# Kernel optimization log

Measured on AMD Instinct MI355X. Metric: run time of the kernel, lower is better.

The kernel has to match this reference:

```python
import jax, jax.numpy as jnp
import numpy as np

DEPTH = 6
HEADS = 4
DH = 64
MAXLEN = 512

def layer_norm(x, s, b, eps=1e-5):
    m = jnp.mean(x, axis=-1, keepdims=True)
    v = jnp.var(x, axis=-1, keepdims=True)
    return (x - m) / jnp.sqrt(v + eps) * s + b

def setup_inputs() -> dict:
    key = jax.random.key(0)
    ks = jax.random.split(key, 8)
    D = 256
    inner = HEADS * DH  # 256
    hid = 1024          # int(256 * 4.0)
    init = lambda k, shape: jax.random.normal(k, shape, jnp.float32) * 0.02
    return {
        "x": jax.random.normal(ks[0], (8, 12, 512, 256), jnp.float32),
        "ln1_s": jnp.ones((DEPTH, D), jnp.float32), "ln1_b": jnp.zeros((DEPTH, D), jnp.float32),
        "qkv_w": init(ks[1], (DEPTH, D, 3 * inner)), "qkv_b": jnp.zeros((DEPTH, 3 * inner), jnp.float32),
        "proj_w": init(ks[2], (DEPTH, inner, D)), "proj_b": jnp.zeros((DEPTH, D), jnp.float32),
        "rel_table": init(ks[3], (DEPTH, 2 * MAXLEN - 1, HEADS)),
        "ln2_s": jnp.ones((DEPTH, D), jnp.float32), "ln2_b": jnp.zeros((DEPTH, D), jnp.float32),
        "w1": init(ks[4], (DEPTH, D, hid)), "b1": jnp.zeros((DEPTH, hid), jnp.float32),
        "w2": init(ks[5], (DEPTH, hid, D)), "b2": jnp.zeros((DEPTH, D), jnp.float32),
        "lnf_s": jnp.ones((D,), jnp.float32), "lnf_b": jnp.zeros((D,), jnp.float32),
    }

def reference(x, ln1_s, ln1_b, qkv_w, qkv_b, proj_w, proj_b, rel_table,
              ln2_s, ln2_b, w1, b1, w2, b2, lnf_s, lnf_b):
    B, L, N, D = x.shape
    h = x.reshape(B * L, N, D)  # (b l) n d
    idx = jnp.arange(N)
    rel_idx = idx[:, None] - idx[None, :] + MAXLEN - 1  # (N, N) in [0, 2*MAXLEN-2]
    scale = DH ** -0.5
    for d in range(DEPTH):
        # pre-norm attention with relative position bias
        xn = layer_norm(h, ln1_s[d], ln1_b[d])
        qkv = xn @ qkv_w[d] + qkv_b[d]
        q, k, v = jnp.split(qkv, 3, axis=-1)
        split_heads = lambda t: t.reshape(B * L, N, HEADS, DH).transpose(0, 2, 1, 3)
        q, k, v = split_heads(q), split_heads(k), split_heads(v)
        bias = rel_table[d][rel_idx].transpose(2, 0, 1)  # (H, N, N)
        scores = jnp.einsum('bhid,bhjd->bhij', q, k) * scale + bias[None]
        attn = jax.nn.softmax(scores, axis=-1)
        o = jnp.einsum('bhij,bhjd->bhid', attn, v)
        o = o.transpose(0, 2, 1, 3).reshape(B * L, N, HEADS * DH)
        h = h + (o @ proj_w[d] + proj_b[d])
        # pre-norm FFN
        xn2 = layer_norm(h, ln2_s[d], ln2_b[d])
        h = h + (jax.nn.gelu(xn2 @ w1[d] + b1[d]) @ w2[d] + b2[d])
    h = layer_norm(h, lnf_s, lnf_b)
    return h.reshape(B, L, N, D)
```

## Files before the change

### kernel.cpp

```cpp
#include <hip/hip_runtime.h>
#include <math.h>

#define T_TOK 49152
#define DMODEL 256
#define NSEQ 512
#define BLROWS 96

typedef unsigned short ushortT;
using frag_ab = __attribute__((ext_vector_type(8))) short;
using f32x4   = __attribute__((ext_vector_type(4))) float;

__device__ __forceinline__ ushortT f2b(float f) {
    union { float f; unsigned int u; } v; v.f = f;
    unsigned int u = v.u;
    u += 0x7FFFu + ((u >> 16) & 1u);
    return (ushortT)(u >> 16);
}
__device__ __forceinline__ float b2f(ushortT h) {
    union { unsigned int u; float f; } v; v.u = ((unsigned int)h) << 16;
    return v.f;
}

__device__ __forceinline__ void gload_lds16(const ushortT* g, ushortT* l) {
    __builtin_amdgcn_global_load_lds(
        (const __attribute__((address_space(1))) unsigned int*)g,
        (__attribute__((address_space(3))) unsigned int*)l, 16, 0, 0);
}

__global__ __launch_bounds__(256) void wprep_kernel(const float* __restrict__ qkv_w,
                                                    const float* __restrict__ proj_w,
                                                    const float* __restrict__ w1,
                                                    const float* __restrict__ w2,
                                                    ushortT* __restrict__ out) {
    __shared__ float Ls[64][132];
    int bid = blockIdx.x;
    int d = bid / 96, t = bid % 96;
    const float* src; int N, KS; size_t dbase; int tt;
    if (t < 24)      { src = qkv_w  + (size_t)d * 256 * 768;  N = 768;  KS = 4;  dbase = (size_t)d * 196608;            tt = t;      }
    else if (t < 32) { src = proj_w + (size_t)d * 256 * 256;  N = 256;  KS = 4;  dbase = 1179648 + (size_t)d * 65536;   tt = t - 24; }
    else if (t < 64) { src = w1     + (size_t)d * 256 * 1024; N = 1024; KS = 4;  dbase = 1572864 + (size_t)d * 262144;  tt = t - 32; }
    else             { src = w2     + (size_t)d * 1024 * 256; N = 256;  KS = 16; dbase = 3145728 + (size_t)d * 262144;  tt = t - 64; }
    int nb = tt / KS, ks = tt % KS;
    int k0 = ks * 64, n0 = nb * 128;
    int tid = threadIdx.x;
#pragma unroll
    for (int i = 0; i < 8; ++i) {
        int fidx = tid + i * 256;
        int kk = fidx >> 5, ng = fidx & 31;
        float4 v = *(const float4*)(src + (size_t)(k0 + kk) * N + n0 + ng * 4);
        *(float4*)&Ls[kk][ng * 4] = v;
    }
    __syncthreads();
    int n = tid & 127, kh = tid >> 7;
    ushortT* dst = out + dbase + (size_t)tt * 8192 + n * 64 + kh * 32;
    ushortT tmp[32];
#pragma unroll
    for (int j = 0; j < 32; ++j) tmp[j] = f2b(Ls[kh * 32 + j][n]);
#pragma unroll
    for (int u = 0; u < 4; ++u) *(uint4*)(dst + u * 8) = *(uint4*)(tmp + u * 8);
}

template <bool OB>
__global__ __launch_bounds__(256) void ln_kernel(const float* __restrict__ in,
                                                 void* __restrict__ out,
                                                 const float* __restrict__ s,
                                                 const float* __restrict__ b) {
    int wave = threadIdx.x >> 6;
    int lane = threadIdx.x & 63;
    size_t row = (size_t)blockIdx.x * 4 + wave;
    float4 v = reinterpret_cast<const float4*>(in + row * DMODEL)[lane];
    float sum = v.x + v.y + v.z + v.w;
    float ssq = v.x * v.x + v.y * v.y + v.z * v.z + v.w * v.w;
#pragma unroll
    for (int m = 1; m <= 32; m <<= 1) {
        sum += __shfl_xor(sum, m, 64);
        ssq += __shfl_xor(ssq, m, 64);
    }
    float mean = sum * (1.0f / 256.0f);
    float var = ssq * (1.0f / 256.0f) - mean * mean;
    float rstd = rsqrtf(var + 1e-5f);
    float4 sv = reinterpret_cast<const float4*>(s)[lane];
    float4 bv = reinterpret_cast<const float4*>(b)[lane];
    float o0 = (v.x - mean) * rstd * sv.x + bv.x;
    float o1 = (v.y - mean) * rstd * sv.y + bv.y;
    float o2 = (v.z - mean) * rstd * sv.z + bv.z;
    float o3 = (v.w - mean) * rstd * sv.w + bv.w;
    if (OB) {
        ushortT* po = (ushortT*)out + row * DMODEL + lane * 4;
        ushort4 ov; ov.x = f2b(o0); ov.y = f2b(o1); ov.z = f2b(o2); ov.w = f2b(o3);
        *(ushort4*)po = ov;
    } else {
        float4 ov; ov.x = o0; ov.y = o1; ov.z = o2; ov.w = o3;
        reinterpret_cast<float4*>((float*)out + row * DMODEL)[lane] = ov;
    }
}

template <int EPI>
__global__ __launch_bounds__(256) void gemm_bf16(const ushortT* __restrict__ A,
                                                 const ushortT* __restrict__ Wt,
                                                 const float* __restrict__ bias,
                                                 float* __restrict__ R,
                                                 ushortT* __restrict__ Cb,
                                                 int K, int N) {
    __shared__ ushortT smem[32768];
    const int nb = blockIdx.x, n0 = nb * 128;
    const int m0 = blockIdx.y * 128;
    const int tid = threadIdx.x, lane = tid & 63, wave = tid >> 6;
    const int wr = wave >> 1, wc = wave & 1;
    const int KS = K >> 6;
    const size_t wtile = (size_t)nb * KS * 8192;

    const int rA = lane >> 3;
    const int colsw = (lane & 7) ^ rA;

    auto STAGE = [&](int buf, int kt) {
        ushortT* Ad = smem + buf * 16384;
        ushortT* Bd = Ad + 8192;
#pragma unroll
        for (int c2 = 0; c2 < 4; ++c2) {
            int rb = wave * 32 + c2 * 8;
            int row = rb + rA;
            gload_lds16(A + (size_t)(m0 + row) * K + kt * 64 + colsw * 8,
                        Ad + rb * 64);
            gload_lds16(Wt + wtile + (size_t)kt * 8192 + row * 64 + colsw * 8,
                        Bd + rb * 64);
        }
    };

    f32x4 acc[4][4];
#pragma unroll
    for (int i = 0; i < 4; ++i)
#pragma unroll
        for (int j = 0; j < 4; ++j) acc[i][j] = (f32x4)0.0f;

    STAGE(0, 0);
    __syncthreads();
    int cur = 0;
    for (int kt = 0; kt < KS; ++kt) {
        if (kt + 1 < KS) STAGE(cur ^ 1, kt + 1);
        const ushortT* Ab = smem + cur * 16384;
        const ushortT* Bb = Ab + 8192;
#pragma unroll
        for (int kst = 0; kst < 2; ++kst) {
            frag_ab af[4], bf4[4];
            int ku = kst * 4 + (lane >> 4);
#pragma unroll
            for (int f = 0; f < 4; ++f) {
                int row = wr * 64 + f * 16 + (lane & 15);
                af[f] = *(const frag_ab*)&Ab[row * 64 + ((ku ^ (row & 7)) << 3)];
                int col = wc * 64 + f * 16 + (lane & 15);
                bf4[f] = *(const frag_ab*)&Bb[col * 64 + ((ku ^ (col & 7)) << 3)];
            }
#pragma unroll
            for (int mf = 0; mf < 4; ++mf)
#pragma unroll
                for (int nf = 0; nf < 4; ++nf)
                    acc[mf][nf] = __builtin_amdgcn_mfma_f32_16x16x32_bf16(
                        af[mf], bf4[nf], acc[mf][nf], 0, 0, 0);
        }
        __syncthreads();
        cur ^= 1;
    }

    const int cg = lane >> 4, cl = lane & 15;
    if (EPI != 2) {
        ushortT* Cs = smem;
#pragma unroll
        for (int nf = 0; nf < 4; ++nf) {
            int col = wc * 64 + nf * 16 + cl;
            float bv = bias[n0 + col];
#pragma unroll
            for (int mf = 0; mf < 4; ++mf)
#pragma unroll
                for (int r = 0; r < 4; ++r) {
                    int row = wr * 64 + mf * 16 + cg * 4 + r;
                    float c = acc[mf][nf][r] + bv;
                    if (EPI == 1) {
                        c = c / (1.0f + __expf(-1.5957691216f * (c + 0.044715f * c * c * c)));
                    }
                    Cs[row * 128 + (((col >> 3) ^ (row & 7)) << 3) + (col & 7)] = f2b(c);
                }
        }
        __syncthreads();
#pragma unroll
        for (int it = 0; it < 8; ++it) {
            int idx = tid + it * 256;
            int row = idx >> 4, u = idx & 15;
            uint4 v = *(uint4*)&Cs[row * 128 + ((u ^ (row & 7)) << 3)];
            *(uint4*)&Cb[(size_t)(m0 + row) * N + n0 + u * 8] = v;
        }
    } else {
        float* Cf = (float*)smem;
#pragma unroll
        for (int h = 0; h < 2; ++h) {
            if (wr == h) {
#pragma unroll
                for (int nf = 0; nf < 4; ++nf) {
                    int col = wc * 64 + nf * 16 + cl;
                    float bv = bias[n0 + col];
#pragma unroll
                    for (int mf = 0; mf < 4; ++mf)
#pragma unroll
                        for (int r = 0; r < 4; ++r) {
                            int rl = mf * 16 + cg * 4 + r;
                            Cf[rl * 128 + (((col >> 2) ^ (rl & 7)) << 2) + (col & 3)] =
                                acc[mf][nf][r] + bv;
                        }
                }
            }
            __syncthreads();
#pragma unroll
            for (int it = 0; it < 8; ++it) {
                int idx = tid + it * 256;
                int row2 = idx >> 5, u = idx & 31;
                float4 c4 = *(float4*)&Cf[row2 * 128 + ((u ^ (row2 & 7)) << 2)];
                float* rp = R + (size_t)(m0 + h * 64 + row2) * N + n0 + u * 4;
                float4 r4 = *(float4*)rp;
                r4.x += c4.x; r4.y += c4.y; r4.z += c4.z; r4.w += c4.w;
                *(float4*)rp = r4;
            }
            if (h == 0) __syncthreads();
        }
    }
}

__global__ __launch_bounds__(256) void attn_kernel(const ushortT* __restrict__ qkv,
                                                   const float* __restrict__ rel,
                                                   ushortT* __restrict__ o) {
    __shared__ ushortT Ks[64 * 64];
    __shared__ ushortT Vt[64 * 72];
    __shared__ ushortT Ps[64 * 64];
    __shared__ float   rl[1024];

    const int pair = blockIdx.x, qb = blockIdx.y;
    const int bl = pair >> 2, hh = pair & 3;
    const int tid = threadIdx.x;
    const int lane = tid & 63, w = tid >> 6;
    const int c15 = lane & 15, g = lane >> 4;
    const size_t base = (size_t)bl * NSEQ * 768;
    const int qoff = hh * 64, koff = 256 + hh * 64, voff = 512 + hh * 64;
    const int i0 = qb * 64;

    for (int i = tid; i < 1023; i += 256) rl[i] = rel[(size_t)i * 4 + hh];

    frag_ab qf[2];
    {
        const ushortT* qp = qkv + base + (size_t)(i0 + w * 16 + c15) * 768 + qoff + g * 8;
        qf[0] = *(const frag_ab*)(qp);
        qf[1] = *(const frag_ab*)(qp + 32);
    }

    float m_i[4], l_i[4];
    f32x4 oacc[4];
#pragma unroll
    for (int r = 0; r < 4; ++r) { m_i[r] = -1e30f; l_i[r] = 0.0f; }
#pragma unroll
    for (int nf = 0; nf < 4; ++nf) oacc[nf] = (f32x4)0.0f;

    const int irow = w * 16 + g * 4;

    for (int kt = 0; kt < 8; ++kt) {
        __syncthreads();
#pragma unroll
        for (int it = 0; it < 2; ++it) {
            int idx = tid + it * 256;
            int j = idx >> 3, dg = idx & 7;
            const ushortT* kp = qkv + base + (size_t)(kt * 64 + j) * 768;
            uint4 kv4 = *(const uint4*)(kp + koff + dg * 8);
            *(uint4*)&Ks[j * 64 + ((dg ^ (j & 7)) << 3)] = kv4;
            uint4 vv4 = *(const uint4*)(kp + voff + dg * 8);
            ushortT tmp[8];
            *(uint4*)tmp = vv4;
            int jc = j ^ (dg << 3);
#pragma unroll
            for (int e = 0; e < 8; ++e) Vt[(dg * 8 + e) * 72 + jc] = tmp[e];
        }
        __syncthreads();

        f32x4 sacc[4];
#pragma unroll
        for (int nf = 0; nf < 4; ++nf) sacc[nf] = (f32x4)0.0f;
#pragma unroll
        for (int kst = 0; kst < 2; ++kst) {
            int ku = kst * 4 + g;
#pragma unroll
            for (int nf = 0; nf < 4; ++nf) {
                int j = nf * 16 + c15;
                frag_ab kf = *(frag_ab*)&Ks[j * 64 + ((ku ^ (j & 7)) << 3)];
                sacc[nf] = __builtin_amdgcn_mfma_f32_16x16x32_bf16(qf[kst], kf, sacc[nf], 0, 0, 0);
            }
        }

        float sv[4][4];
        const int rlb = i0 + irow - kt * 64 - c15 + 511;
#pragma unroll
        for (int nf = 0; nf < 4; ++nf)
#pragma unroll
            for (int r = 0; r < 4; ++r)
                sv[nf][r] = sacc[nf][r] * 0.125f + rl[rlb + r - nf * 16];

        float corr[4], psum[4];
        unsigned int words[4][4];
#pragma unroll
        for (int r = 0; r < 4; ++r) {
            float rmax = fmaxf(fmaxf(sv[0][r], sv[1][r]), fmaxf(sv[2][r], sv[3][r]));
#pragma unroll
            for (int m = 1; m <= 8; m <<= 1) rmax = fmaxf(rmax, __shfl_xor(rmax, m, 64));
            float mn = fmaxf(m_i[r], rmax);
            corr[r] = __expf(m_i[r] - mn);
            m_i[r] = mn;
            psum[r] = 0.0f;
        }
#pragma unroll
        for (int nf = 0; nf < 4; ++nf)
#pragma unroll
            for (int r = 0; r < 4; ++r) {
                float p = __expf(sv[nf][r] - m_i[r]);
                psum[r] += p;
                unsigned int own = (unsigned int)f2b(p);
                unsigned int other = (unsigned int)__shfl_xor((int)own, 1, 64);
                words[nf][r] = own | (other << 16);
            }
#pragma unroll
        for (int r = 0; r < 4; ++r) {
#pragma unroll
            for (int m = 1; m <= 8; m <<= 1) psum[r] += __shfl_xor(psum[r], m, 64);
            l_i[r] = l_i[r] * corr[r] + psum[r];
        }

        if (!(lane & 1)) {
#pragma unroll
            for (int nf = 0; nf < 4; ++nf) {
                int j2 = nf * 16 + c15;
#pragma unroll
                for (int r = 0; r < 4; ++r) {
                    int i = irow + r;
                    *(unsigned int*)&Ps[i * 64 + ((((j2 >> 3) ^ (i & 7))) << 3) + (j2 & 7)] =
                        words[nf][r];
                }
            }
        }

#pragma unroll
        for (int nf = 0; nf < 4; ++nf)
#pragma unroll
            for (int r = 0; r < 4; ++r) oacc[nf][r] *= corr[r];

#pragma unroll
        for (int ks2 = 0; ks2 < 2; ++ks2) {
            int ip = w * 16 + c15;
            int jb = ks2 * 32 + g * 8;
            frag_ab pf = *(frag_ab*)&Ps[ip * 64 + (((jb >> 3) ^ (ip & 7)) << 3)];
#pragma unroll
            for (int nf = 0; nf < 4; ++nf) {
                int dh = nf * 16 + c15;
                int jv = jb ^ ((dh >> 3) << 3);
                frag_ab vf = *(frag_ab*)&Vt[dh * 72 + jv];
                oacc[nf] = __builtin_amdgcn_mfma_f32_16x16x32_bf16(pf, vf, oacc[nf], 0, 0, 0);
            }
        }
    }

    float inv[4];
#pragma unroll
    for (int r = 0; r < 4; ++r) inv[r] = 1.0f / l_i[r];
#pragma unroll
    for (int nf = 0; nf < 4; ++nf)
#pragma unroll
        for (int r = 0; r < 4; ++r) {
            unsigned int own = (unsigned int)f2b(oacc[nf][r] * inv[r]);
            unsigned int other = (unsigned int)__shfl_xor((int)own, 1, 64);
            if (!(lane & 1)) {
                size_t trow = (size_t)bl * NSEQ + i0 + irow + r;
                *(unsigned int*)&o[trow * DMODEL + hh * 64 + nf * 16 + c15] = own | (other << 16);
            }
        }
}

extern "C" void kernel_launch(void* const* d_in, const int* in_sizes, int n_in,
                              void* d_out, int out_size, void* d_ws, size_t ws_size,
                              hipStream_t stream) {
    const float* x       = (const float*)d_in[0];
    const float* ln1_s   = (const float*)d_in[1];
    const float* ln1_b   = (const float*)d_in[2];
    const float* qkv_w   = (const float*)d_in[3];
    const float* qkv_b   = (const float*)d_in[4];
    const float* proj_w  = (const float*)d_in[5];
    const float* proj_b  = (const float*)d_in[6];
    const float* rel_tab = (const float*)d_in[7];
    const float* ln2_s   = (const float*)d_in[8];
    const float* ln2_b   = (const float*)d_in[9];
    const float* w1      = (const float*)d_in[10];
    const float* b1      = (const float*)d_in[11];
    const float* w2      = (const float*)d_in[12];
    const float* b2      = (const float*)d_in[13];
    const float* lnf_s   = (const float*)d_in[14];
    const float* lnf_b   = (const float*)d_in[15];

    float* h = (float*)d_out;
    ushortT* wsu = (ushortT*)d_ws;
    const size_t WPRE = 4718592;

    static const int cands[12] = {1, 2, 3, 4, 6, 8, 12, 16, 24, 32, 48, 96};
    int NC = 96;
    for (int i = 0; i < 12; ++i) {
        size_t tc = (size_t)T_TOK / cands[i];
        if (WPRE * 2 + tc * 3072 <= ws_size) { NC = cands[i]; break; }
    }
    const int TC = T_TOK / NC;
    const int BLC = BLROWS / NC;
    ushortT* xnC = wsu + WPRE;
    ushortT* big = xnC + (size_t)TC * 256;
    ushortT* oC  = big + (size_t)TC * 1024;

    wprep_kernel<<<576, 256, 0, stream>>>(qkv_w, proj_w, w1, w2, wsu);
    hipMemcpyAsync(h, x, (size_t)T_TOK * DMODEL * sizeof(float),
                   hipMemcpyDeviceToDevice, stream);

    dim3 blk(256);
    for (int d = 0; d < 6; ++d) {
        for (int c = 0; c < NC; ++c) {
            float* hc = h + (size_t)c * TC * DMODEL;
            ln_kernel<true><<<TC / 4, blk, 0, stream>>>(hc, xnC, ln1_s + d * 256, ln1_b + d * 256);
            gemm_bf16<0><<<dim3(6, TC / 128), blk, 0, stream>>>(
                xnC, wsu + (size_t)d * 196608, qkv_b + d * 768, nullptr, big, 256, 768);
            attn_kernel<<<dim3(BLC * 4, NSEQ / 64), blk, 0, stream>>>(
                big, rel_tab + (size_t)d * 1023 * 4, oC);
            gemm_bf16<2><<<dim3(2, TC / 128), blk, 0, stream>>>(
                oC, wsu + 1179648 + (size_t)d * 65536, proj_b + d * 256, hc, nullptr, 256, 256);
        }
        for (int c = 0; c < NC; ++c) {
            float* hc = h + (size_t)c * TC * DMODEL;
            ln_kernel<true><<<TC / 4, blk, 0, stream>>>(hc, xnC, ln2_s + d * 256, ln2_b + d * 256);
            gemm_bf16<1><<<dim3(8, TC / 128), blk, 0, stream>>>(
                xnC, wsu + 1572864 + (size_t)d * 262144, b1 + d * 1024, nullptr, big, 256, 1024);
            gemm_bf16<2><<<dim3(2, TC / 128), blk, 0, stream>>>(
                big, wsu + 3145728 + (size_t)d * 262144, b2 + d * 256, hc, nullptr, 1024, 256);
        }
    }
    ln_kernel<false><<<T_TOK / 4, blk, 0, stream>>>(h, h, lnf_s, lnf_b);
}
```

Measured before the change: 2.161 ms.

## Widen attention blocks to 128 queries, use exp2 and lazy rescale

The attention kernel now runs 512 threads per block and covers 128 query rows, so each K/V tile staged into shared memory serves twice as many queries and the per-block staging loop drops to one iteration per thread. Softmax moves to base-2 exponentials, with log2e folded into the scale and the bias table. The running-max rescale of the accumulators is skipped when the whole wave's new max stays within a threshold of the old one. Packing to bf16 now uses the hardware v_cvt_pk_bf16_f32 instruction instead of manual rounding and integer shuffles. The trade-offs are more shared memory and threads per block, fewer blocks in the grid, and partial sums that can grow larger before renormalisation.

```diff
diff --git a/kernel.cpp b/kernel.cpp
--- a/kernel.cpp
+++ b/kernel.cpp
@@ -5,6 +5,7 @@
 #define DMODEL 256
 #define NSEQ 512
 #define BLROWS 96
+#define LOG2E 1.4426950408889634f
 
 typedef unsigned short ushortT;
 using frag_ab = __attribute__((ext_vector_type(8))) short;
@@ -19,6 +20,18 @@
 __device__ __forceinline__ float b2f(ushortT h) {
     union { unsigned int u; float f; } v; v.u = ((unsigned int)h) << 16;
     return v.f;
+}
+
+#if __has_builtin(__builtin_amdgcn_exp2f)
+#define FEXP2(x) __builtin_amdgcn_exp2f(x)
+#else
+#define FEXP2(x) __expf((x) * 0.6931471805599453f)
+#endif
+
+__device__ __forceinline__ unsigned int cvtpk_bf16(float lo, float hi) {
+    unsigned int r;
+    asm("v_cvt_pk_bf16_f32 %0, %1, %2" : "=v"(r) : "v"(lo), "v"(hi));
+    return r;
 }
 
 __device__ __forceinline__ void gload_lds16(const ushortT* g, ushortT* l) {
@@ -224,12 +237,12 @@
     }
 }
 
-__global__ __launch_bounds__(256) void attn_kernel(const ushortT* __restrict__ qkv,
+__global__ __launch_bounds__(512) void attn_kernel(const ushortT* __restrict__ qkv,
                                                    const float* __restrict__ rel,
                                                    ushortT* __restrict__ o) {
     __shared__ ushortT Ks[64 * 64];
     __shared__ ushortT Vt[64 * 72];
-    __shared__ ushortT Ps[64 * 64];
+    __shared__ ushortT Ps[128 * 64];
     __shared__ float   rl[1024];
 
     const int pair = blockIdx.x, qb = blockIdx.y;
@@ -239,9 +252,9 @@
     const int c15 = lane & 15, g = lane >> 4;
     const size_t base = (size_t)bl * NSEQ * 768;
     const int qoff = hh * 64, koff = 256 + hh * 64, voff = 512 + hh * 64;
-    const int i0 = qb * 64;
-
-    for (int i = tid; i < 1023; i += 256) rl[i] = rel[(size_t)i * 4 + hh];
+    const int i0 = qb * 128;
+
+    for (int i = tid; i < 1023; i += 512) rl[i] = rel[(size_t)i * 4 + hh] * LOG2E;
 
     frag_ab qf[2];
     {
@@ -261,10 +274,8 @@
 
     for (int kt = 0; kt < 8; ++kt) {
         __syncthreads();
-#pragma unroll
-        for (int it = 0; it < 2; ++it) {
-            int idx = tid + it * 256;
-            int j = idx >> 3, dg = idx & 7;
+        {
+            int j = tid >> 3, dg = tid & 7;
             const ushortT* kp = qkv + base + (size_t)(kt * 64 + j) * 768;
             uint4 kv4 = *(const uint4*)(kp + koff + dg * 8);
             *(uint4*)&Ks[j * 64 + ((dg ^ (j & 7)) << 3)] = kv4;
@@ -297,35 +308,47 @@
         for (int nf = 0; nf < 4; ++nf)
 #pragma unroll
             for (int r = 0; r < 4; ++r)
-                sv[nf][r] = sacc[nf][r] * 0.125f + rl[rlb + r - nf * 16];
-
-        float corr[4], psum[4];
+                sv[nf][r] = sacc[nf][r] * (0.125f * LOG2E) + rl[rlb + r - nf * 16];
+
+        float rmax[4];
+#pragma unroll
+        for (int r = 0; r < 4; ++r) {
+            float rm = fmaxf(fmaxf(sv[0][r], sv[1][r]), fmaxf(sv[2][r], sv[3][r]));
+#pragma unroll
+            for (int m = 1; m <= 8; m <<= 1) rm = fmaxf(rm, __shfl_xor(rm, m, 64));
+            rmax[r] = rm;
+        }
+        bool cskip = true;
+#pragma unroll
+        for (int r = 0; r < 4; ++r) cskip = cskip && (rmax[r] <= m_i[r] + 11.5f);
+        if (!__all(cskip)) {
+#pragma unroll
+            for (int r = 0; r < 4; ++r) {
+                float mn = fmaxf(m_i[r], rmax[r]);
+                float cr = FEXP2(m_i[r] - mn);
+                m_i[r] = mn;
+                l_i[r] *= cr;
+#pragma unroll
+                for (int nf = 0; nf < 4; ++nf) oacc[nf][r] *= cr;
+            }
+        }
+
+        float psum[4] = {0.0f, 0.0f, 0.0f, 0.0f};
         unsigned int words[4][4];
 #pragma unroll
+        for (int nf = 0; nf < 4; ++nf)
+#pragma unroll
+            for (int r = 0; r < 4; ++r) {
+                float p = FEXP2(sv[nf][r] - m_i[r]);
+                psum[r] += p;
+                float po = __shfl_xor(p, 1, 64);
+                words[nf][r] = cvtpk_bf16(p, po);
+            }
+#pragma unroll
         for (int r = 0; r < 4; ++r) {
-            float rmax = fmaxf(fmaxf(sv[0][r], sv[1][r]), fmaxf(sv[2][r], sv[3][r]));
-#pragma unroll
-            for (int m = 1; m <= 8; m <<= 1) rmax = fmaxf(rmax, __shfl_xor(rmax, m, 64));
-            float mn = fmaxf(m_i[r], rmax);
-            corr[r] = __expf(m_i[r] - mn);
-            m_i[r] = mn;
-            psum[r] = 0.0f;
-        }
-#pragma unroll
-        for (int nf = 0; nf < 4; ++nf)
-#pragma unroll
-            for (int r = 0; r < 4; ++r) {
-                float p = __expf(sv[nf][r] - m_i[r]);
-                psum[r] += p;
-                unsigned int own = (unsigned int)f2b(p);
-                unsigned int other = (unsigned int)__shfl_xor((int)own, 1, 64);
-                words[nf][r] = own | (other << 16);
-            }
-#pragma unroll
-        for (int r = 0; r < 4; ++r) {
 #pragma unroll
             for (int m = 1; m <= 8; m <<= 1) psum[r] += __shfl_xor(psum[r], m, 64);
-            l_i[r] = l_i[r] * corr[r] + psum[r];
+            l_i[r] += psum[r];
         }
 
         if (!(lane & 1)) {
@@ -342,11 +365,6 @@
         }
 
 #pragma unroll
-        for (int nf = 0; nf < 4; ++nf)
-#pragma unroll
-            for (int r = 0; r < 4; ++r) oacc[nf][r] *= corr[r];
-
-#pragma unroll
         for (int ks2 = 0; ks2 < 2; ++ks2) {
             int ip = w * 16 + c15;
             int jb = ks2 * 32 + g * 8;
@@ -368,11 +386,12 @@
     for (int nf = 0; nf < 4; ++nf)
 #pragma unroll
         for (int r = 0; r < 4; ++r) {
-            unsigned int own = (unsigned int)f2b(oacc[nf][r] * inv[r]);
-            unsigned int other = (unsigned int)__shfl_xor((int)own, 1, 64);
+            float own = oacc[nf][r] * inv[r];
+            float other = __shfl_xor(own, 1, 64);
             if (!(lane & 1)) {
                 size_t trow = (size_t)bl * NSEQ + i0 + irow + r;
-                *(unsigned int*)&o[trow * DMODEL + hh * 64 + nf * 16 + c15] = own | (other << 16);
+                *(unsigned int*)&o[trow * DMODEL + hh * 64 + nf * 16 + c15] =
+                    cvtpk_bf16(own, other);
             }
         }
 }
@@ -424,7 +443,7 @@
             ln_kernel<true><<<TC / 4, blk, 0, stream>>>(hc, xnC, ln1_s + d * 256, ln1_b + d * 256);
             gemm_bf16<0><<<dim3(6, TC / 128), blk, 0, stream>>>(
                 xnC, wsu + (size_t)d * 196608, qkv_b + d * 768, nullptr, big, 256, 768);
-            attn_kernel<<<dim3(BLC * 4, NSEQ / 64), blk, 0, stream>>>(
+            attn_kernel<<<dim3(BLC * 4, NSEQ / 128), 512, 0, stream>>>(
                 big, rel_tab + (size_t)d * 1023 * 4, oC);
             gemm_bf16<2><<<dim3(2, TC / 128), blk, 0, stream>>>(
                 oC, wsu + 1179648 + (size_t)d * 65536, proj_b + d * 256, hc, nullptr, 256, 256);
```

After: 2.051 ms. 5.1% less time.
